# Kernel tuning notes

Measured on AMD Instinct MI355X. Metric: run time of the kernel, lower is better.

The kernel has to match this reference:

```python
import jax, jax.numpy as jnp
import numpy as np
import math

N_HEADS = 16

def _apply_rope(t, cos, sin):
    # t: [b, h, s, hd]; cos/sin: [s, hd//2] (interleaved pairs, llama2.c style)
    b, h, s, hd = t.shape
    tr = t.reshape(b, h, s, hd // 2, 2)
    x_r, x_i = tr[..., 0], tr[..., 1]
    c = cos[None, None, :, :]
    sn = sin[None, None, :, :]
    o_r = x_r * c - x_i * sn
    o_i = x_r * sn + x_i * c
    return jnp.stack([o_r, o_i], axis=-1).reshape(b, h, s, hd)

def setup_inputs() -> dict:
    key = jax.random.key(0)
    ks = jax.random.split(key, 7)
    b, s, d = 4, 2048, 2048
    hd = d // N_HEADS
    x = jax.random.normal(ks[0], (b, s, d), dtype=jnp.float32)
    # RoPE tables: cos/sin of theta * pos, standard 10000 base
    inv_freq = 1.0 / (10000.0 ** (np.arange(0, hd, 2, dtype=np.float32) / hd))
    pos = np.arange(s, dtype=np.float32)
    ang = np.outer(pos, inv_freq)  # [s, hd/2]
    freq_cos = jnp.asarray(np.cos(ang), dtype=jnp.float32)
    freq_sin = jnp.asarray(np.sin(ang), dtype=jnp.float32)
    Wqkv = jax.random.normal(ks[1], (d, 3 * d), dtype=jnp.float32) * (1.0 / math.sqrt(d))
    bqkv = jnp.zeros((3 * d,), dtype=jnp.float32)
    Wout = jax.random.normal(ks[2], (d, d), dtype=jnp.float32) * (1.0 / math.sqrt(d))
    bout = jnp.zeros((d,), dtype=jnp.float32)
    return {"x": x, "freq_cos": freq_cos, "freq_sin": freq_sin,
            "Wqkv": Wqkv, "bqkv": bqkv, "Wout": Wout, "bout": bout}

def reference(x, freq_cos, freq_sin, Wqkv, bqkv, Wout, bout):
    b, s, d = x.shape
    hd = d // N_HEADS
    qkv = x @ Wqkv + bqkv                       # [b, s, 3d]
    q, k, v = jnp.split(qkv, 3, axis=-1)
    def to_heads(t):
        return t.reshape(b, s, N_HEADS, hd).transpose(0, 2, 1, 3)  # [b, h, s, hd]
    q, k, v = to_heads(q), to_heads(k), to_heads(v)
    q = _apply_rope(q, freq_cos, freq_sin)
    k = _apply_rope(k, freq_cos, freq_sin)
    att = jnp.einsum('bhqd,bhkd->bhqk', q, k) / math.sqrt(hd)
    mask = jnp.tril(jnp.ones((s, s), dtype=bool))
    att = jnp.where(mask[None, None, :, :], att, -jnp.inf)
    att = jax.nn.softmax(att, axis=-1)
    y = jnp.einsum('bhqk,bhkd->bhqd', att, v)
    y = y.transpose(0, 2, 1, 3).reshape(b, s, d)
    return y @ Wout + bout
```

## Files before the change

kernel.cpp:

```cpp
#include <hip/hip_runtime.h>

typedef __attribute__((ext_vector_type(4))) float f32x4;
typedef __attribute__((ext_vector_type(8))) short bf16x8;
typedef __attribute__((ext_vector_type(4))) unsigned int uint4v;
typedef __attribute__((ext_vector_type(4))) unsigned short ushort4v;
typedef unsigned short u16;
typedef unsigned int u32;

#define AS1(p) ((const __attribute__((address_space(1))) u32*)(p))
#define AS3(p) ((__attribute__((address_space(3))) u32*)(p))

__device__ __forceinline__ float bf2f(u16 v) {
    u32 u = ((u32)v) << 16;
    return __builtin_bit_cast(float, u);
}
__device__ __forceinline__ u16 f2bf(float f) {
    u32 u = __builtin_bit_cast(u32, f);
    u += 0x7fffu + ((u >> 16) & 1u);
    return (u16)(u >> 16);
}

__global__ __launch_bounds__(256) void k_cvt_bf16(const float* __restrict__ in,
                                                  u16* __restrict__ out, int n8) {
    int t = blockIdx.x * 256 + threadIdx.x;
    if (t >= n8) return;
    const f32x4* p = (const f32x4*)in + (size_t)t * 2;
    f32x4 a = p[0], b = p[1];
    uint4v o;
    o[0] = (u32)f2bf(a[0]) | ((u32)f2bf(a[1]) << 16);
    o[1] = (u32)f2bf(a[2]) | ((u32)f2bf(a[3]) << 16);
    o[2] = (u32)f2bf(b[0]) | ((u32)f2bf(b[1]) << 16);
    o[3] = (u32)f2bf(b[2]) | ((u32)f2bf(b[3]) << 16);
    *((uint4v*)(out + (size_t)t * 8)) = o;
}

__global__ __launch_bounds__(256) void k_transpose_bf16(const float* __restrict__ in,
                                                        u16* __restrict__ out,
                                                        int R, int C) {
    __shared__ float tile[32][33];
    const int bx = blockIdx.x * 32, by = blockIdx.y * 32;
    const int tx = threadIdx.x & 31, ty = threadIdx.x >> 5;
#pragma unroll
    for (int i = 0; i < 32; i += 8)
        tile[ty + i][tx] = in[(size_t)(by + ty + i) * C + bx + tx];
    __syncthreads();
#pragma unroll
    for (int i = 0; i < 32; i += 8)
        out[(size_t)(bx + ty + i) * R + by + tx] = f2bf(tile[tx][ty + i]);
}

template <int OUT_BF16>
__global__ __launch_bounds__(512, 2) void k_gemm256(const u16* __restrict__ A,
                                                    const u16* __restrict__ Bt,
                                                    const float* __restrict__ bias,
                                                    void* __restrict__ Cout,
                                                    int M, int N, int K) {
    __shared__ u16 lds[65536];
    const int tid = threadIdx.x;
    const int wid = tid >> 6, l = tid & 63;
    const int lr = l & 15, lg = l >> 4;
    const int wm = wid >> 2, wn = wid & 3;
    const size_t brow = (size_t)blockIdx.x * 256;
    const size_t bcol = (size_t)blockIdx.y * 256;
    const int KT = K >> 5;

    const int srow = l & 15, scol = (l >> 4) * 8;
    const u16* gA0 = A  + (brow + (size_t)(2 * wid)     * 16 + srow) * K + scol;
    const u16* gA1 = A  + (brow + (size_t)(2 * wid + 1) * 16 + srow) * K + scol;
    const u16* gB0 = Bt + (bcol + (size_t)(2 * wid)     * 16 + srow) * K + scol;
    const u16* gB1 = Bt + (bcol + (size_t)(2 * wid + 1) * 16 + srow) * K + scol;

    f32x4 acc[8][4];
#pragma unroll
    for (int m = 0; m < 8; ++m)
#pragma unroll
        for (int n = 0; n < 4; ++n) acc[m][n] = (f32x4){0.f, 0.f, 0.f, 0.f};

#define STAGE(t)                                                                   \
    {                                                                              \
        const int b_ = (t) & 3;                                                    \
        const int k0_ = (t) << 5;                                                  \
        u16* dA_ = &lds[b_ * 8192 + (2 * wid) * 512];                              \
        u16* dB_ = &lds[32768 + b_ * 8192 + (2 * wid) * 512];                      \
        __builtin_amdgcn_global_load_lds(AS1(gA0 + k0_), AS3(dA_), 16, 0, 0);      \
        __builtin_amdgcn_global_load_lds(AS1(gA1 + k0_), AS3(dA_ + 512), 16, 0, 0);\
        __builtin_amdgcn_global_load_lds(AS1(gB0 + k0_), AS3(dB_), 16, 0, 0);      \
        __builtin_amdgcn_global_load_lds(AS1(gB1 + k0_), AS3(dB_ + 512), 16, 0, 0);\
    }

    STAGE(0); STAGE(1); STAGE(2);
    asm volatile("s_waitcnt vmcnt(8)" ::: "memory");
    __builtin_amdgcn_s_barrier();
    __builtin_amdgcn_sched_barrier(0);

#pragma unroll 1
    for (int t = 0; t < KT; ++t) {
        if (t + 3 < KT) STAGE(t + 3);
        const u16* pa = &lds[(t & 3) * 8192 + wm * 4096 + lg * 128 + lr * 8];
        const u16* pb = &lds[32768 + (t & 3) * 8192 + wn * 2048 + lg * 128 + lr * 8];
        bf16x8 af[8], bf[4];
#pragma unroll
        for (int m = 0; m < 8; ++m) af[m] = *(const bf16x8*)(pa + m * 512);
#pragma unroll
        for (int n = 0; n < 4; ++n) bf[n] = *(const bf16x8*)(pb + n * 512);
        __builtin_amdgcn_s_setprio(1);
#pragma unroll
        for (int m = 0; m < 8; ++m)
#pragma unroll
            for (int n = 0; n < 4; ++n)
                acc[m][n] = __builtin_amdgcn_mfma_f32_16x16x32_bf16(af[m], bf[n], acc[m][n], 0, 0, 0);
        __builtin_amdgcn_s_setprio(0);
        __builtin_amdgcn_sched_barrier(0);
        if (t < KT - 3)       asm volatile("s_waitcnt vmcnt(8)" ::: "memory");
        else if (t == KT - 3) asm volatile("s_waitcnt vmcnt(4)" ::: "memory");
        else if (t == KT - 2) asm volatile("s_waitcnt vmcnt(0)" ::: "memory");
        if (t < KT - 1) __builtin_amdgcn_s_barrier();
        __builtin_amdgcn_sched_barrier(0);
    }
#undef STAGE

    const int crow0 = wm * 128 + lg * 4;
    const int ccol0 = wn * 64 + lr;
#pragma unroll
    for (int m = 0; m < 8; ++m) {
        const size_t row0 = brow + crow0 + m * 16;
#pragma unroll
        for (int n = 0; n < 4; ++n) {
            const size_t col = bcol + ccol0 + n * 16;
            const float bv = bias[col];
#pragma unroll
            for (int r = 0; r < 4; ++r) {
                float v = acc[m][n][r] + bv;
                if (OUT_BF16)
                    ((u16*)Cout)[(row0 + r) * N + col] = f2bf(v);
                else
                    ((float*)Cout)[(row0 + r) * N + col] = v;
            }
        }
    }
}

__global__ __launch_bounds__(256) void k_rope(const u16* __restrict__ qkv,
                                              const float* __restrict__ fcos,
                                              const float* __restrict__ fsin,
                                              u16* __restrict__ qb, u16* __restrict__ kb) {
    const int t = blockIdx.x * 256 + threadIdx.x;
    const int e = t & 7, h = (t >> 3) & 15, r = (t >> 7) & 1, s = (t >> 8) & 2047, b = t >> 19;
    const u16* src = qkv + ((size_t)(b * 2048 + s)) * 6144 + r * 2048 + h * 128 + e * 16;
    uint4v p0 = *(const uint4v*)src;
    uint4v p1 = *(const uint4v*)(src + 8);
    const float* cp = fcos + s * 64 + e * 8;
    const float* sp = fsin + s * 64 + e * 8;
    f32x4 c0 = *(const f32x4*)cp, c1 = *(const f32x4*)(cp + 4);
    f32x4 s0 = *(const f32x4*)sp, s1 = *(const f32x4*)(sp + 4);
    float x[16];
#pragma unroll
    for (int i = 0; i < 4; ++i) {
        x[2 * i]     = bf2f((u16)(p0[i] & 0xffff));
        x[2 * i + 1] = bf2f((u16)(p0[i] >> 16));
        x[8 + 2 * i]     = bf2f((u16)(p1[i] & 0xffff));
        x[8 + 2 * i + 1] = bf2f((u16)(p1[i] >> 16));
    }
    float c[8]  = {c0[0], c0[1], c0[2], c0[3], c1[0], c1[1], c1[2], c1[3]};
    float sn[8] = {s0[0], s0[1], s0[2], s0[3], s1[0], s1[1], s1[2], s1[3]};
    u32 ow[8];
#pragma unroll
    for (int i = 0; i < 8; ++i) {
        float xr = x[2 * i], xi = x[2 * i + 1];
        float orr = xr * c[i] - xi * sn[i];
        float oii = xr * sn[i] + xi * c[i];
        ow[i] = (u32)f2bf(orr) | ((u32)f2bf(oii) << 16);
    }
    u16* dst = (r ? kb : qb) + ((size_t)((b * 16 + h) * 2048 + s)) * 128 + e * 16;
    uint4v q0 = {ow[0], ow[1], ow[2], ow[3]};
    uint4v q1 = {ow[4], ow[5], ow[6], ow[7]};
    *(uint4v*)dst = q0;
    *(uint4v*)(dst + 8) = q1;
}

struct VtRegs { uint4v v0, v1, v2, v3; };

__device__ __forceinline__ void attn_stage_k(const u16* kp, int kbase, u16* dstBase,
                                             int w, int lr, int lg) {
#pragma unroll
    for (int c = 0; c < 4; ++c) {
        const int row = w * 16 + c * 4 + lg;
        const int sslot = lr ^ (4 * (c & 1) + lg);
        const u16* gsrc = kp + (size_t)(kbase + row) * 128 + sslot * 8;
        __builtin_amdgcn_global_load_lds(AS1(gsrc), AS3(dstBase + (w * 16 + c * 4) * 128), 16, 0, 0);
    }
}

__device__ __forceinline__ VtRegs attn_load_v(const u16* vp, int kbase, int tid) {
    const int rg = tid >> 4, cg = tid & 15;
    const u16* gv = vp + (size_t)(kbase + rg * 4) * 6144 + cg * 8;
    VtRegs r;
    r.v0 = *(const uint4v*)gv;
    r.v1 = *(const uint4v*)(gv + 6144);
    r.v2 = *(const uint4v*)(gv + 2 * 6144);
    r.v3 = *(const uint4v*)(gv + 3 * 6144);
    return r;
}

__device__ __forceinline__ void attn_write_v(u16 (*Vt)[64], const VtRegs& r, int tid) {
    const int rg = tid >> 4, cg = tid & 15;
    const u16* u0 = (const u16*)&r.v0;
    const u16* u1 = (const u16*)&r.v1;
    const u16* u2 = (const u16*)&r.v2;
    const u16* u3 = (const u16*)&r.v3;
    const int sb = rg >> 1, hf = (rg & 1) * 4;
#pragma unroll
    for (int cc = 0; cc < 8; ++cc) {
        const int row = cg * 8 + cc;
        const int col = ((sb ^ ((cg ^ cc) & 7)) << 3) + hf;
        ushort4v pk = {u0[cc], u1[cc], u2[cc], u3[cc]};
        *(ushort4v*)&Vt[row][col] = pk;
    }
}

__device__ __forceinline__ void attn_qtile(int qt, const u16* qp, const u16* kp,
                                           const u16* vp, u16* yp,
                                           u16 (*Ks)[64][128], u16 (*Vt)[64],
                                           u16 (*Psw)[72],
                                           int w, int lr, int lg, int tid) {
    const int qw = qt * 128 + w * 32;

    bf16x8 qf[2][4];
#pragma unroll
    for (int i = 0; i < 2; ++i)
#pragma unroll
        for (int ks = 0; ks < 4; ++ks)
            qf[i][ks] = *(const bf16x8*)(qp + (size_t)(qw + i * 16 + lr) * 128 + ks * 32 + lg * 8);

    f32x4 acc[2][8];
#pragma unroll
    for (int i = 0; i < 2; ++i)
#pragma unroll
        for (int j = 0; j < 8; ++j) acc[i][j] = (f32x4){0.f, 0.f, 0.f, 0.f};
    float mrow[2][4], lrow[2][4];
#pragma unroll
    for (int i = 0; i < 2; ++i)
#pragma unroll
        for (int r = 0; r < 4; ++r) { mrow[i][r] = -1e30f; lrow[i][r] = 0.f; }

    const float scale = 0.08838834764831845f;
    const int nkt = 2 * qt + 2;

    attn_stage_k(kp, 0, &Ks[0][0][0], w, lr, lg);
    VtRegs vr = attn_load_v(vp, 0, tid);
    attn_write_v(Vt, vr, tid);
    __syncthreads();

    int cur = 0;
    for (int kt = 0; kt < nkt; ++kt) {
        const int kbase = kt * 64;
        const bool pf = (kt + 1 < nkt);
        if (pf) {
            attn_stage_k(kp, kbase + 64, &Ks[cur ^ 1][0][0], w, lr, lg);
            vr = attn_load_v(vp, kbase + 64, tid);
        }

        if (kbase <= qw + 31) {
            f32x4 sc[2][4];
#pragma unroll
            for (int i = 0; i < 2; ++i)
#pragma unroll
                for (int j = 0; j < 4; ++j) sc[i][j] = (f32x4){0.f, 0.f, 0.f, 0.f};
#pragma unroll
            for (int nt = 0; nt < 4; ++nt) {
#pragma unroll
                for (int ks = 0; ks < 4; ++ks) {
                    const int slot = (ks * 4 + lg) ^ (lr & 7);
                    bf16x8 kf = *(const bf16x8*)&Ks[cur][nt * 16 + lr][slot * 8];
#pragma unroll
                    for (int mt = 0; mt < 2; ++mt)
                        sc[mt][nt] = __builtin_amdgcn_mfma_f32_16x16x32_bf16(qf[mt][ks], kf, sc[mt][nt], 0, 0, 0);
                }
            }
            const bool pm = (kbase + 63 > qw);
#pragma unroll
            for (int mt = 0; mt < 2; ++mt)
#pragma unroll
                for (int nt = 0; nt < 4; ++nt)
#pragma unroll
                    for (int r = 0; r < 4; ++r) {
                        float v = sc[mt][nt][r] * scale;
                        if (pm) {
                            const int qi = qw + mt * 16 + lg * 4 + r;
                            const int ki = kbase + nt * 16 + lr;
                            if (ki > qi) v = -1e30f;
                        }
                        sc[mt][nt][r] = v;
                    }
            float rm[2][4];
#pragma unroll
            for (int mt = 0; mt < 2; ++mt)
#pragma unroll
                for (int r = 0; r < 4; ++r)
                    rm[mt][r] = fmaxf(fmaxf(sc[mt][0][r], sc[mt][1][r]),
                                      fmaxf(sc[mt][2][r], sc[mt][3][r]));
#pragma unroll
            for (int off = 8; off; off >>= 1)
#pragma unroll
                for (int mt = 0; mt < 2; ++mt)
#pragma unroll
                    for (int r = 0; r < 4; ++r)
                        rm[mt][r] = fmaxf(rm[mt][r], __shfl_xor(rm[mt][r], off, 16));
            float fac[2][4];
#pragma unroll
            for (int mt = 0; mt < 2; ++mt)
#pragma unroll
                for (int r = 0; r < 4; ++r) {
                    const float mn = fmaxf(mrow[mt][r], rm[mt][r]);
                    fac[mt][r] = __expf(mrow[mt][r] - mn);
                    mrow[mt][r] = mn;
                    lrow[mt][r] *= fac[mt][r];
                }
#pragma unroll
            for (int mt = 0; mt < 2; ++mt)
#pragma unroll
                for (int nt = 0; nt < 8; ++nt)
#pragma unroll
                    for (int r = 0; r < 4; ++r) acc[mt][nt][r] *= fac[mt][r];
            float rs[2][4] = {{0.f, 0.f, 0.f, 0.f}, {0.f, 0.f, 0.f, 0.f}};
#pragma unroll
            for (int mt = 0; mt < 2; ++mt)
#pragma unroll
                for (int nt = 0; nt < 4; ++nt)
#pragma unroll
                    for (int r = 0; r < 4; ++r) {
                        const float p = __expf(sc[mt][nt][r] - mrow[mt][r]);
                        sc[mt][nt][r] = p;
                        rs[mt][r] += p;
                    }
#pragma unroll
            for (int off = 8; off; off >>= 1)
#pragma unroll
                for (int mt = 0; mt < 2; ++mt)
#pragma unroll
                    for (int r = 0; r < 4; ++r)
                        rs[mt][r] += __shfl_xor(rs[mt][r], off, 16);
#pragma unroll
            for (int mt = 0; mt < 2; ++mt)
#pragma unroll
                for (int r = 0; r < 4; ++r) lrow[mt][r] += rs[mt][r];
#pragma unroll
            for (int mt = 0; mt < 2; ++mt)
#pragma unroll
                for (int nt = 0; nt < 4; ++nt)
#pragma unroll
                    for (int r = 0; r < 4; ++r)
                        Psw[mt * 16 + lg * 4 + r][nt * 16 + lr] = f2bf(sc[mt][nt][r]);
#pragma unroll
            for (int k2 = 0; k2 < 2; ++k2) {
                bf16x8 pa[2];
                pa[0] = *(const bf16x8*)&Psw[lr][k2 * 32 + lg * 8];
                pa[1] = *(const bf16x8*)&Psw[16 + lr][k2 * 32 + lg * 8];
#pragma unroll
                for (int nt = 0; nt < 8; ++nt) {
                    const int f = ((nt * 2 + (lr >> 3)) ^ lr) & 7;
                    const int slot = (k2 * 4 + lg) ^ f;
                    bf16x8 vb = *(const bf16x8*)&Vt[nt * 16 + lr][slot * 8];
#pragma unroll
                    for (int mt = 0; mt < 2; ++mt)
                        acc[mt][nt] = __builtin_amdgcn_mfma_f32_16x16x32_bf16(pa[mt], vb, acc[mt][nt], 0, 0, 0);
                }
            }
        }

        __syncthreads();
        if (pf) attn_write_v(Vt, vr, tid);
        __syncthreads();
        cur ^= 1;
    }

#pragma unroll
    for (int mt = 0; mt < 2; ++mt)
#pragma unroll
        for (int r = 0; r < 4; ++r) {
            const float inv = 1.f / lrow[mt][r];
            const size_t row = qw + mt * 16 + lg * 4 + r;
#pragma unroll
            for (int nt = 0; nt < 8; ++nt)
                yp[row * 2048 + nt * 16 + lr] = f2bf(acc[mt][nt][r] * inv);
        }
}

__global__ __launch_bounds__(256, 2) void k_attn(const u16* __restrict__ qb,
                                                 const u16* __restrict__ kb,
                                                 const u16* __restrict__ qkv,
                                                 u16* __restrict__ yb) {
    __shared__ u16 Ks[2][64][128];
    __shared__ u16 Vt[128][64];
    __shared__ u16 Ps[4][32][72];

    const int gid = blockIdx.x;
    const int x = gid >> 6;
    const int g = gid & 63;
    const int h = g & 15, b = g >> 4;
    const int tid = threadIdx.x;
    const int w = tid >> 6, l = tid & 63;
    const int lr = l & 15, lg = l >> 4;

    const u16* qp = qb + (size_t)((b * 16 + h) * 2048) * 128;
    const u16* kp = kb + (size_t)((b * 16 + h) * 2048) * 128;
    const u16* vp = qkv + (size_t)(b * 2048) * 6144 + 4096 + h * 128;
    u16* yp = yb + (size_t)(b * 2048) * 2048 + h * 128;

    attn_qtile(x,      qp, kp, vp, yp, Ks, Vt, Ps[w], w, lr, lg, tid);
    attn_qtile(15 - x, qp, kp, vp, yp, Ks, Vt, Ps[w], w, lr, lg, tid);
}

extern "C" void kernel_launch(void* const* d_in, const int* in_sizes, int n_in,
                              void* d_out, int out_size, void* d_ws, size_t ws_size,
                              hipStream_t stream) {
    const float* x    = (const float*)d_in[0];
    const float* fcos = (const float*)d_in[1];
    const float* fsin = (const float*)d_in[2];
    const float* Wqkv = (const float*)d_in[3];
    const float* bqkv = (const float*)d_in[4];
    const float* Wout = (const float*)d_in[5];
    const float* bout = (const float*)d_in[6];
    float* out = (float*)d_out;

    if (ws_size < 234881024u) return;

    char* ws = (char*)d_ws;
    u16* x_bf  = (u16*)(ws);
    u16* wqkvT = (u16*)(ws + 33554432);
    u16* woutT = (u16*)(ws + 58720256);
    u16* qkv   = (u16*)(ws + 67108864);
    u16* qb    = (u16*)(ws + 167772160);
    u16* kb    = (u16*)(ws + 201326592);
    u16* yb    = x_bf;

    k_cvt_bf16<<<8192, 256, 0, stream>>>(x, x_bf, 2097152);
    k_transpose_bf16<<<dim3(192, 64), 256, 0, stream>>>(Wqkv, wqkvT, 2048, 6144);
    k_transpose_bf16<<<dim3(64, 64), 256, 0, stream>>>(Wout, woutT, 2048, 2048);
    k_gemm256<1><<<dim3(32, 24), 512, 0, stream>>>(x_bf, wqkvT, bqkv, qkv, 8192, 6144, 2048);
    k_rope<<<8192, 256, 0, stream>>>(qkv, fcos, fsin, qb, kb);
    k_attn<<<512, 256, 0, stream>>>(qb, kb, qkv, yb);
    k_gemm256<0><<<dim3(32, 8), 512, 0, stream>>>(yb, woutT, bout, out, 8192, 2048, 2048);
}
```

Measured before the change: 555.7 us.

## Use 32x32 MFMA in GEMM and lazy rescaling with exp2 in attention

Rewrites the 256x256 GEMM tile to use 32x32x16 bf16 MFMAs with a new LDS staging layout, splitting the MFMA block into two halves around barriers, which reduces LDS fragment reads per FLOP. In the attention softmax it folds log2(e) into the scale, uses exp2f, and skips the online-softmax rescale of the accumulator unless the running max grows by more than a threshold (lazy rescaling). The GEMM change reorganizes the schedule and adds an extra barrier per iteration. Lazy rescaling risks precision only if skipped growth leads to large exponents, which the threshold bounds.

```diff
diff --git a/kernel.cpp b/kernel.cpp
--- a/kernel.cpp
+++ b/kernel.cpp
@@ -1,6 +1,7 @@
 #include <hip/hip_runtime.h>
 
 typedef __attribute__((ext_vector_type(4))) float f32x4;
+typedef __attribute__((ext_vector_type(16))) float f32x16;
 typedef __attribute__((ext_vector_type(8))) short bf16x8;
 typedef __attribute__((ext_vector_type(4))) unsigned int uint4v;
 typedef __attribute__((ext_vector_type(4))) unsigned short ushort4v;
@@ -58,34 +59,33 @@
     __shared__ u16 lds[65536];
     const int tid = threadIdx.x;
     const int wid = tid >> 6, l = tid & 63;
-    const int lr = l & 15, lg = l >> 4;
     const int wm = wid >> 2, wn = wid & 3;
     const size_t brow = (size_t)blockIdx.x * 256;
     const size_t bcol = (size_t)blockIdx.y * 256;
     const int KT = K >> 5;
 
-    const int srow = l & 15, scol = (l >> 4) * 8;
-    const u16* gA0 = A  + (brow + (size_t)(2 * wid)     * 16 + srow) * K + scol;
-    const u16* gA1 = A  + (brow + (size_t)(2 * wid + 1) * 16 + srow) * K + scol;
-    const u16* gB0 = Bt + (bcol + (size_t)(2 * wid)     * 16 + srow) * K + scol;
-    const u16* gB1 = Bt + (bcol + (size_t)(2 * wid + 1) * 16 + srow) * K + scol;
-
-    f32x4 acc[8][4];
-#pragma unroll
-    for (int m = 0; m < 8; ++m)
-#pragma unroll
-        for (int n = 0; n < 4; ++n) acc[m][n] = (f32x4){0.f, 0.f, 0.f, 0.f};
-
-#define STAGE(t)                                                                   \
-    {                                                                              \
-        const int b_ = (t) & 3;                                                    \
-        const int k0_ = (t) << 5;                                                  \
-        u16* dA_ = &lds[b_ * 8192 + (2 * wid) * 512];                              \
-        u16* dB_ = &lds[32768 + b_ * 8192 + (2 * wid) * 512];                      \
-        __builtin_amdgcn_global_load_lds(AS1(gA0 + k0_), AS3(dA_), 16, 0, 0);      \
-        __builtin_amdgcn_global_load_lds(AS1(gA1 + k0_), AS3(dA_ + 512), 16, 0, 0);\
-        __builtin_amdgcn_global_load_lds(AS1(gB0 + k0_), AS3(dB_), 16, 0, 0);      \
-        __builtin_amdgcn_global_load_lds(AS1(gB1 + k0_), AS3(dB_ + 512), 16, 0, 0);\
+    const int srow = l & 31, sk8 = (l >> 5) * 8;
+    const u16* gA = A  + (brow + (size_t)wid * 32 + srow) * K + sk8;
+    const u16* gB = Bt + (bcol + (size_t)wid * 32 + srow) * K + sk8;
+
+    f32x16 acc[4][2];
+#pragma unroll
+    for (int m = 0; m < 4; ++m)
+#pragma unroll
+        for (int n = 0; n < 2; ++n)
+#pragma unroll
+            for (int r = 0; r < 16; ++r) acc[m][n][r] = 0.f;
+
+#define STAGE(t)                                                                       \
+    {                                                                                  \
+        const int b_ = (t) & 3;                                                        \
+        const int k0_ = (t) << 5;                                                      \
+        u16* dA_ = &lds[b_ * 8192 + wid * 1024];                                       \
+        u16* dB_ = &lds[32768 + b_ * 8192 + wid * 1024];                               \
+        __builtin_amdgcn_global_load_lds(AS1(gA + k0_), AS3(dA_), 16, 0, 0);           \
+        __builtin_amdgcn_global_load_lds(AS1(gA + k0_ + 16), AS3(dA_ + 512), 16, 0, 0);\
+        __builtin_amdgcn_global_load_lds(AS1(gB + k0_), AS3(dB_), 16, 0, 0);           \
+        __builtin_amdgcn_global_load_lds(AS1(gB + k0_ + 16), AS3(dB_ + 512), 16, 0, 0);\
     }
 
     STAGE(0); STAGE(1); STAGE(2);
@@ -96,45 +96,65 @@
 #pragma unroll 1
     for (int t = 0; t < KT; ++t) {
         if (t + 3 < KT) STAGE(t + 3);
-        const u16* pa = &lds[(t & 3) * 8192 + wm * 4096 + lg * 128 + lr * 8];
-        const u16* pb = &lds[32768 + (t & 3) * 8192 + wn * 2048 + lg * 128 + lr * 8];
-        bf16x8 af[8], bf[4];
-#pragma unroll
-        for (int m = 0; m < 8; ++m) af[m] = *(const bf16x8*)(pa + m * 512);
-#pragma unroll
-        for (int n = 0; n < 4; ++n) bf[n] = *(const bf16x8*)(pb + n * 512);
-        __builtin_amdgcn_s_setprio(1);
-#pragma unroll
-        for (int m = 0; m < 8; ++m)
-#pragma unroll
-            for (int n = 0; n < 4; ++n)
-                acc[m][n] = __builtin_amdgcn_mfma_f32_16x16x32_bf16(af[m], bf[n], acc[m][n], 0, 0, 0);
-        __builtin_amdgcn_s_setprio(0);
-        __builtin_amdgcn_sched_barrier(0);
+        const u16* pa = &lds[(t & 3) * 8192 + wm * 4096 + l * 8];
+        const u16* pb = &lds[32768 + (t & 3) * 8192 + wn * 2048 + l * 8];
+        bf16x8 af[4][2], bf[2][2];
+#pragma unroll
+        for (int m = 0; m < 4; ++m)
+#pragma unroll
+            for (int h = 0; h < 2; ++h)
+                af[m][h] = *(const bf16x8*)(pa + m * 1024 + h * 512);
+#pragma unroll
+        for (int n = 0; n < 2; ++n)
+#pragma unroll
+            for (int h = 0; h < 2; ++h)
+                bf[n][h] = *(const bf16x8*)(pb + n * 1024 + h * 512);
         if (t < KT - 3)       asm volatile("s_waitcnt vmcnt(8)" ::: "memory");
         else if (t == KT - 3) asm volatile("s_waitcnt vmcnt(4)" ::: "memory");
         else if (t == KT - 2) asm volatile("s_waitcnt vmcnt(0)" ::: "memory");
-        if (t < KT - 1) __builtin_amdgcn_s_barrier();
+        __builtin_amdgcn_s_barrier();
         __builtin_amdgcn_sched_barrier(0);
+        __builtin_amdgcn_s_setprio(1);
+#pragma unroll
+        for (int m = 0; m < 2; ++m)
+#pragma unroll
+            for (int n = 0; n < 2; ++n)
+#pragma unroll
+                for (int h = 0; h < 2; ++h)
+                    acc[m][n] = __builtin_amdgcn_mfma_f32_32x32x16_bf16(af[m][h], bf[n][h], acc[m][n], 0, 0, 0);
+        __builtin_amdgcn_s_setprio(0);
+        __builtin_amdgcn_s_barrier();
+        __builtin_amdgcn_sched_barrier(0);
+        __builtin_amdgcn_s_setprio(1);
+#pragma unroll
+        for (int m = 2; m < 4; ++m)
+#pragma unroll
+            for (int n = 0; n < 2; ++n)
+#pragma unroll
+                for (int h = 0; h < 2; ++h)
+                    acc[m][n] = __builtin_amdgcn_mfma_f32_32x32x16_bf16(af[m][h], bf[n][h], acc[m][n], 0, 0, 0);
+        __builtin_amdgcn_s_setprio(0);
+        __builtin_amdgcn_sched_barrier(0);
     }
 #undef STAGE
 
-    const int crow0 = wm * 128 + lg * 4;
-    const int ccol0 = wn * 64 + lr;
-#pragma unroll
-    for (int m = 0; m < 8; ++m) {
-        const size_t row0 = brow + crow0 + m * 16;
-#pragma unroll
-        for (int n = 0; n < 4; ++n) {
-            const size_t col = bcol + ccol0 + n * 16;
+    const int rsub = 4 * (l >> 5);
+    const int csub = l & 31;
+#pragma unroll
+    for (int m = 0; m < 4; ++m) {
+        const size_t row0 = brow + wm * 128 + m * 32 + rsub;
+#pragma unroll
+        for (int n = 0; n < 2; ++n) {
+            const size_t col = bcol + wn * 64 + n * 32 + csub;
             const float bv = bias[col];
 #pragma unroll
-            for (int r = 0; r < 4; ++r) {
+            for (int r = 0; r < 16; ++r) {
+                const size_t row = row0 + (r & 3) + 8 * (r >> 2);
                 float v = acc[m][n][r] + bv;
                 if (OUT_BF16)
-                    ((u16*)Cout)[(row0 + r) * N + col] = f2bf(v);
+                    ((u16*)Cout)[row * N + col] = f2bf(v);
                 else
-                    ((float*)Cout)[(row0 + r) * N + col] = v;
+                    ((float*)Cout)[row * N + col] = v;
             }
         }
     }
@@ -243,7 +263,7 @@
 #pragma unroll
         for (int r = 0; r < 4; ++r) { mrow[i][r] = -1e30f; lrow[i][r] = 0.f; }
 
-    const float scale = 0.08838834764831845f;
+    const float scale2 = 0.08838834764831845f * 1.4426950408889634f;
     const int nkt = 2 * qt + 2;
 
     attn_stage_k(kp, 0, &Ks[0][0][0], w, lr, lg);
@@ -284,7 +304,7 @@
                 for (int nt = 0; nt < 4; ++nt)
 #pragma unroll
                     for (int r = 0; r < 4; ++r) {
-                        float v = sc[mt][nt][r] * scale;
+                        float v = sc[mt][nt][r] * scale2;
                         if (pm) {
                             const int qi = qw + mt * 16 + lg * 4 + r;
                             const int ki = kbase + nt * 16 + lr;
@@ -306,22 +326,25 @@
 #pragma unroll
                     for (int r = 0; r < 4; ++r)
                         rm[mt][r] = fmaxf(rm[mt][r], __shfl_xor(rm[mt][r], off, 16));
-            float fac[2][4];
-#pragma unroll
-            for (int mt = 0; mt < 2; ++mt)
-#pragma unroll
-                for (int r = 0; r < 4; ++r) {
-                    const float mn = fmaxf(mrow[mt][r], rm[mt][r]);
-                    fac[mt][r] = __expf(mrow[mt][r] - mn);
-                    mrow[mt][r] = mn;
-                    lrow[mt][r] *= fac[mt][r];
-                }
-#pragma unroll
-            for (int mt = 0; mt < 2; ++mt)
-#pragma unroll
-                for (int nt = 0; nt < 8; ++nt)
-#pragma unroll
-                    for (int r = 0; r < 4; ++r) acc[mt][nt][r] *= fac[mt][r];
+            float mx = -1e30f;
+#pragma unroll
+            for (int mt = 0; mt < 2; ++mt)
+#pragma unroll
+                for (int r = 0; r < 4; ++r)
+                    mx = fmaxf(mx, rm[mt][r] - mrow[mt][r]);
+            if (__any(mx > 11.5f)) {
+#pragma unroll
+                for (int mt = 0; mt < 2; ++mt)
+#pragma unroll
+                    for (int r = 0; r < 4; ++r) {
+                        const float mn = fmaxf(mrow[mt][r], rm[mt][r]);
+                        const float fac = exp2f(mrow[mt][r] - mn);
+                        mrow[mt][r] = mn;
+                        lrow[mt][r] *= fac;
+#pragma unroll
+                        for (int nt = 0; nt < 8; ++nt) acc[mt][nt][r] *= fac;
+                    }
+            }
             float rs[2][4] = {{0.f, 0.f, 0.f, 0.f}, {0.f, 0.f, 0.f, 0.f}};
 #pragma unroll
             for (int mt = 0; mt < 2; ++mt)
@@ -329,7 +352,7 @@
                 for (int nt = 0; nt < 4; ++nt)
 #pragma unroll
                     for (int r = 0; r < 4; ++r) {
-                        const float p = __expf(sc[mt][nt][r] - mrow[mt][r]);
+                        const float p = exp2f(sc[mt][nt][r] - mrow[mt][r]);
                         sc[mt][nt][r] = p;
                         rs[mt][r] += p;
                     }
```

New measurement: 583.2 us. 4.9% more time.

## Restructure GEMM to BK=64 double buffer; transpose attention scores for lane-local softmax

Applied to the files above, without the earlier changes.

The GEMM moves from a 4-stage BK=32 pipeline to a 2-stage BK=64 pipeline, with eight async global-to-LDS loads per stage and two MFMA k-substeps per iteration. This halves the number of barriers per K, but the prefetch depth drops to one stage. In attention, the QK^T MFMA operands are swapped so each lane holds one query row's scores. Row max and sum then need only two cross-lane shuffles, and the rescale factor and final normalizer are gathered with __shfl. The V load is issued before the K stage, and explicit vmcnt/lgkmcnt waits with raw s_barrier replace __syncthreads, so the V global load can overlap the K staging.

```diff
diff --git a/kernel.cpp b/kernel.cpp
--- a/kernel.cpp
+++ b/kernel.cpp
@@ -62,13 +62,17 @@
     const int wm = wid >> 2, wn = wid & 3;
     const size_t brow = (size_t)blockIdx.x * 256;
     const size_t bcol = (size_t)blockIdx.y * 256;
-    const int KT = K >> 5;
-
-    const int srow = l & 15, scol = (l >> 4) * 8;
-    const u16* gA0 = A  + (brow + (size_t)(2 * wid)     * 16 + srow) * K + scol;
-    const u16* gA1 = A  + (brow + (size_t)(2 * wid + 1) * 16 + srow) * K + scol;
-    const u16* gB0 = Bt + (bcol + (size_t)(2 * wid)     * 16 + srow) * K + scol;
-    const u16* gB1 = Bt + (bcol + (size_t)(2 * wid + 1) * 16 + srow) * K + scol;
+    const int KT = K >> 6;
+
+    const u16* gA[4];
+    const u16* gB[4];
+#pragma unroll
+    for (int r = 0; r < 4; ++r) {
+        const int P = r * 8 + wid, g = P >> 1, kh = P & 1;
+        const size_t off = (size_t)(g * 16 + lr) * K + kh * 32 + lg * 8;
+        gA[r] = A + brow * K + off;
+        gB[r] = Bt + bcol * K + off;
+    }
 
     f32x4 acc[8][4];
 #pragma unroll
@@ -76,57 +80,60 @@
 #pragma unroll
         for (int n = 0; n < 4; ++n) acc[m][n] = (f32x4){0.f, 0.f, 0.f, 0.f};
 
-#define STAGE(t)                                                                   \
-    {                                                                              \
-        const int b_ = (t) & 3;                                                    \
-        const int k0_ = (t) << 5;                                                  \
-        u16* dA_ = &lds[b_ * 8192 + (2 * wid) * 512];                              \
-        u16* dB_ = &lds[32768 + b_ * 8192 + (2 * wid) * 512];                      \
-        __builtin_amdgcn_global_load_lds(AS1(gA0 + k0_), AS3(dA_), 16, 0, 0);      \
-        __builtin_amdgcn_global_load_lds(AS1(gA1 + k0_), AS3(dA_ + 512), 16, 0, 0);\
-        __builtin_amdgcn_global_load_lds(AS1(gB0 + k0_), AS3(dB_), 16, 0, 0);      \
-        __builtin_amdgcn_global_load_lds(AS1(gB1 + k0_), AS3(dB_ + 512), 16, 0, 0);\
-    }
-
-    STAGE(0); STAGE(1); STAGE(2);
-    asm volatile("s_waitcnt vmcnt(8)" ::: "memory");
+#define STAGE(t)                                                                        \
+    do {                                                                                \
+        const int b_ = (t) & 1;                                                         \
+        const int k0_ = (t) << 6;                                                       \
+        u16* dA_ = &lds[b_ * 16384];                                                    \
+        u16* dB_ = &lds[32768 + b_ * 16384];                                            \
+        __builtin_amdgcn_global_load_lds(AS1(gA[0] + k0_), AS3(dA_ + (0 * 8 + wid) * 512), 16, 0, 0); \
+        __builtin_amdgcn_global_load_lds(AS1(gB[0] + k0_), AS3(dB_ + (0 * 8 + wid) * 512), 16, 0, 0); \
+        __builtin_amdgcn_global_load_lds(AS1(gA[1] + k0_), AS3(dA_ + (1 * 8 + wid) * 512), 16, 0, 0); \
+        __builtin_amdgcn_global_load_lds(AS1(gB[1] + k0_), AS3(dB_ + (1 * 8 + wid) * 512), 16, 0, 0); \
+        __builtin_amdgcn_global_load_lds(AS1(gA[2] + k0_), AS3(dA_ + (2 * 8 + wid) * 512), 16, 0, 0); \
+        __builtin_amdgcn_global_load_lds(AS1(gB[2] + k0_), AS3(dB_ + (2 * 8 + wid) * 512), 16, 0, 0); \
+        __builtin_amdgcn_global_load_lds(AS1(gA[3] + k0_), AS3(dA_ + (3 * 8 + wid) * 512), 16, 0, 0); \
+        __builtin_amdgcn_global_load_lds(AS1(gB[3] + k0_), AS3(dB_ + (3 * 8 + wid) * 512), 16, 0, 0); \
+    } while (0)
+
+    STAGE(0);
+    asm volatile("s_waitcnt vmcnt(0)" ::: "memory");
     __builtin_amdgcn_s_barrier();
     __builtin_amdgcn_sched_barrier(0);
 
 #pragma unroll 1
     for (int t = 0; t < KT; ++t) {
-        if (t + 3 < KT) STAGE(t + 3);
-        const u16* pa = &lds[(t & 3) * 8192 + wm * 4096 + lg * 128 + lr * 8];
-        const u16* pb = &lds[32768 + (t & 3) * 8192 + wn * 2048 + lg * 128 + lr * 8];
-        bf16x8 af[8], bf[4];
-#pragma unroll
-        for (int m = 0; m < 8; ++m) af[m] = *(const bf16x8*)(pa + m * 512);
-#pragma unroll
-        for (int n = 0; n < 4; ++n) bf[n] = *(const bf16x8*)(pb + n * 512);
-        __builtin_amdgcn_s_setprio(1);
-#pragma unroll
-        for (int m = 0; m < 8; ++m)
-#pragma unroll
-            for (int n = 0; n < 4; ++n)
-                acc[m][n] = __builtin_amdgcn_mfma_f32_16x16x32_bf16(af[m], bf[n], acc[m][n], 0, 0, 0);
-        __builtin_amdgcn_s_setprio(0);
+        if (t + 1 < KT) STAGE(t + 1);
+        const u16* pa = &lds[(t & 1) * 16384 + wm * 8192 + l * 8];
+        const u16* pb = &lds[32768 + (t & 1) * 16384 + wn * 4096 + l * 8];
+#pragma unroll
+        for (int ks = 0; ks < 2; ++ks) {
+            bf16x8 af[8], bfr[4];
+#pragma unroll
+            for (int m = 0; m < 8; ++m) af[m] = *(const bf16x8*)(pa + (m * 2 + ks) * 512);
+#pragma unroll
+            for (int n = 0; n < 4; ++n) bfr[n] = *(const bf16x8*)(pb + (n * 2 + ks) * 512);
+            __builtin_amdgcn_s_setprio(1);
+#pragma unroll
+            for (int m = 0; m < 8; ++m)
+#pragma unroll
+                for (int n = 0; n < 4; ++n)
+                    acc[m][n] = __builtin_amdgcn_mfma_f32_16x16x32_bf16(af[m], bfr[n], acc[m][n], 0, 0, 0);
+            __builtin_amdgcn_s_setprio(0);
+        }
         __builtin_amdgcn_sched_barrier(0);
-        if (t < KT - 3)       asm volatile("s_waitcnt vmcnt(8)" ::: "memory");
-        else if (t == KT - 3) asm volatile("s_waitcnt vmcnt(4)" ::: "memory");
-        else if (t == KT - 2) asm volatile("s_waitcnt vmcnt(0)" ::: "memory");
-        if (t < KT - 1) __builtin_amdgcn_s_barrier();
+        asm volatile("s_waitcnt vmcnt(0)" ::: "memory");
+        __builtin_amdgcn_s_barrier();
         __builtin_amdgcn_sched_barrier(0);
     }
 #undef STAGE
 
-    const int crow0 = wm * 128 + lg * 4;
-    const int ccol0 = wn * 64 + lr;
 #pragma unroll
     for (int m = 0; m < 8; ++m) {
-        const size_t row0 = brow + crow0 + m * 16;
+        const size_t row0 = brow + wm * 128 + m * 16 + lg * 4;
 #pragma unroll
         for (int n = 0; n < 4; ++n) {
-            const size_t col = bcol + ccol0 + n * 16;
+            const size_t col = bcol + wn * 64 + n * 16 + lr;
             const float bv = bias[col];
 #pragma unroll
             for (int r = 0; r < 4; ++r) {
@@ -224,6 +231,7 @@
                                            u16 (*Psw)[72],
                                            int w, int lr, int lg, int tid) {
     const int qw = qt * 128 + w * 32;
+    const int l = tid & 63;
 
     bf16x8 qf[2][4];
 #pragma unroll
@@ -237,17 +245,13 @@
     for (int i = 0; i < 2; ++i)
 #pragma unroll
         for (int j = 0; j < 8; ++j) acc[i][j] = (f32x4){0.f, 0.f, 0.f, 0.f};
-    float mrow[2][4], lrow[2][4];
-#pragma unroll
-    for (int i = 0; i < 2; ++i)
-#pragma unroll
-        for (int r = 0; r < 4; ++r) { mrow[i][r] = -1e30f; lrow[i][r] = 0.f; }
+    float mrow[2] = {-1e30f, -1e30f}, lrow[2] = {0.f, 0.f};
 
     const float scale = 0.08838834764831845f;
     const int nkt = 2 * qt + 2;
 
+    VtRegs vr = attn_load_v(vp, 0, tid);
     attn_stage_k(kp, 0, &Ks[0][0][0], w, lr, lg);
-    VtRegs vr = attn_load_v(vp, 0, tid);
     attn_write_v(Vt, vr, tid);
     __syncthreads();
 
@@ -256,16 +260,16 @@
         const int kbase = kt * 64;
         const bool pf = (kt + 1 < nkt);
         if (pf) {
+            vr = attn_load_v(vp, kbase + 64, tid);
             attn_stage_k(kp, kbase + 64, &Ks[cur ^ 1][0][0], w, lr, lg);
-            vr = attn_load_v(vp, kbase + 64, tid);
         }
 
         if (kbase <= qw + 31) {
-            f32x4 sc[2][4];
+            f32x4 st[2][4];
 #pragma unroll
             for (int i = 0; i < 2; ++i)
 #pragma unroll
-                for (int j = 0; j < 4; ++j) sc[i][j] = (f32x4){0.f, 0.f, 0.f, 0.f};
+                for (int j = 0; j < 4; ++j) st[i][j] = (f32x4){0.f, 0.f, 0.f, 0.f};
 #pragma unroll
             for (int nt = 0; nt < 4; ++nt) {
 #pragma unroll
@@ -274,7 +278,7 @@
                     bf16x8 kf = *(const bf16x8*)&Ks[cur][nt * 16 + lr][slot * 8];
 #pragma unroll
                     for (int mt = 0; mt < 2; ++mt)
-                        sc[mt][nt] = __builtin_amdgcn_mfma_f32_16x16x32_bf16(qf[mt][ks], kf, sc[mt][nt], 0, 0, 0);
+                        st[mt][nt] = __builtin_amdgcn_mfma_f32_16x16x32_bf16(kf, qf[mt][ks], st[mt][nt], 0, 0, 0);
                 }
             }
             const bool pm = (kbase + 63 > qw);
@@ -284,73 +288,67 @@
                 for (int nt = 0; nt < 4; ++nt)
 #pragma unroll
                     for (int r = 0; r < 4; ++r) {
-                        float v = sc[mt][nt][r] * scale;
+                        float v = st[mt][nt][r] * scale;
                         if (pm) {
-                            const int qi = qw + mt * 16 + lg * 4 + r;
-                            const int ki = kbase + nt * 16 + lr;
+                            const int qi = qw + mt * 16 + lr;
+                            const int ki = kbase + nt * 16 + lg * 4 + r;
                             if (ki > qi) v = -1e30f;
                         }
-                        sc[mt][nt][r] = v;
+                        st[mt][nt][r] = v;
                     }
-            float rm[2][4];
+            float rm[2], fac[2];
+#pragma unroll
+            for (int mt = 0; mt < 2; ++mt) {
+                float m0 = st[mt][0][0];
+#pragma unroll
+                for (int nt = 0; nt < 4; ++nt)
+#pragma unroll
+                    for (int r = 0; r < 4; ++r) m0 = fmaxf(m0, st[mt][nt][r]);
+                m0 = fmaxf(m0, __shfl_xor(m0, 16));
+                m0 = fmaxf(m0, __shfl_xor(m0, 32));
+                rm[mt] = m0;
+                const float mn = fmaxf(mrow[mt], m0);
+                fac[mt] = __expf(mrow[mt] - mn);
+                mrow[mt] = mn;
+                lrow[mt] *= fac[mt];
+            }
+            float facr[2][4];
 #pragma unroll
             for (int mt = 0; mt < 2; ++mt)
 #pragma unroll
                 for (int r = 0; r < 4; ++r)
-                    rm[mt][r] = fmaxf(fmaxf(sc[mt][0][r], sc[mt][1][r]),
-                                      fmaxf(sc[mt][2][r], sc[mt][3][r]));
-#pragma unroll
-            for (int off = 8; off; off >>= 1)
-#pragma unroll
-                for (int mt = 0; mt < 2; ++mt)
-#pragma unroll
-                    for (int r = 0; r < 4; ++r)
-                        rm[mt][r] = fmaxf(rm[mt][r], __shfl_xor(rm[mt][r], off, 16));
-            float fac[2][4];
+                    facr[mt][r] = __shfl(fac[mt], (l & 48) | (lg * 4 + r));
 #pragma unroll
             for (int mt = 0; mt < 2; ++mt)
 #pragma unroll
-                for (int r = 0; r < 4; ++r) {
-                    const float mn = fmaxf(mrow[mt][r], rm[mt][r]);
-                    fac[mt][r] = __expf(mrow[mt][r] - mn);
-                    mrow[mt][r] = mn;
-                    lrow[mt][r] *= fac[mt][r];
+                for (int nt = 0; nt < 8; ++nt)
+#pragma unroll
+                    for (int r = 0; r < 4; ++r) acc[mt][nt][r] *= facr[mt][r];
+#pragma unroll
+            for (int mt = 0; mt < 2; ++mt) {
+                float rs = 0.f;
+#pragma unroll
+                for (int nt = 0; nt < 4; ++nt)
+#pragma unroll
+                    for (int r = 0; r < 4; ++r) {
+                        const float p = __expf(st[mt][nt][r] - mrow[mt]);
+                        st[mt][nt][r] = p;
+                        rs += p;
+                    }
+                rs += __shfl_xor(rs, 16);
+                rs += __shfl_xor(rs, 32);
+                lrow[mt] += rs;
+            }
+#pragma unroll
+            for (int mt = 0; mt < 2; ++mt)
+#pragma unroll
+                for (int nt = 0; nt < 4; ++nt) {
+                    const u32 p01 = (u32)f2bf(st[mt][nt][0]) | ((u32)f2bf(st[mt][nt][1]) << 16);
+                    const u32 p23 = (u32)f2bf(st[mt][nt][2]) | ((u32)f2bf(st[mt][nt][3]) << 16);
+                    u16* dst = &Psw[mt * 16 + lr][nt * 16 + lg * 4];
+                    *(u32*)dst = p01;
+                    *(u32*)(dst + 2) = p23;
                 }
-#pragma unroll
-            for (int mt = 0; mt < 2; ++mt)
-#pragma unroll
-                for (int nt = 0; nt < 8; ++nt)
-#pragma unroll
-                    for (int r = 0; r < 4; ++r) acc[mt][nt][r] *= fac[mt][r];
-            float rs[2][4] = {{0.f, 0.f, 0.f, 0.f}, {0.f, 0.f, 0.f, 0.f}};
-#pragma unroll
-            for (int mt = 0; mt < 2; ++mt)
-#pragma unroll
-                for (int nt = 0; nt < 4; ++nt)
-#pragma unroll
-                    for (int r = 0; r < 4; ++r) {
-                        const float p = __expf(sc[mt][nt][r] - mrow[mt][r]);
-                        sc[mt][nt][r] = p;
-                        rs[mt][r] += p;
-                    }
-#pragma unroll
-            for (int off = 8; off; off >>= 1)
-#pragma unroll
-                for (int mt = 0; mt < 2; ++mt)
-#pragma unroll
-                    for (int r = 0; r < 4; ++r)
-                        rs[mt][r] += __shfl_xor(rs[mt][r], off, 16);
-#pragma unroll
-            for (int mt = 0; mt < 2; ++mt)
-#pragma unroll
-                for (int r = 0; r < 4; ++r) lrow[mt][r] += rs[mt][r];
-#pragma unroll
-            for (int mt = 0; mt < 2; ++mt)
-#pragma unroll
-                for (int nt = 0; nt < 4; ++nt)
-#pragma unroll
-                    for (int r = 0; r < 4; ++r)
-                        Psw[mt * 16 + lg * 4 + r][nt * 16 + lr] = f2bf(sc[mt][nt][r]);
 #pragma unroll
             for (int k2 = 0; k2 < 2; ++k2) {
                 bf16x8 pa[2];
@@ -368,9 +366,17 @@
             }
         }
 
-        __syncthreads();
-        if (pf) attn_write_v(Vt, vr, tid);
-        __syncthreads();
+        __builtin_amdgcn_s_barrier();
+        __builtin_amdgcn_sched_barrier(0);
+        if (pf) {
+            asm volatile("s_waitcnt vmcnt(4)" ::: "memory");
+            attn_write_v(Vt, vr, tid);
+            asm volatile("s_waitcnt vmcnt(0) lgkmcnt(0)" ::: "memory");
+        } else {
+            asm volatile("s_waitcnt vmcnt(0) lgkmcnt(0)" ::: "memory");
+        }
+        __builtin_amdgcn_s_barrier();
+        __builtin_amdgcn_sched_barrier(0);
         cur ^= 1;
     }
 
@@ -378,7 +384,8 @@
     for (int mt = 0; mt < 2; ++mt)
 #pragma unroll
         for (int r = 0; r < 4; ++r) {
-            const float inv = 1.f / lrow[mt][r];
+            const float lsum = __shfl(lrow[mt], (l & 48) | (lg * 4 + r));
+            const float inv = 1.f / lsum;
             const size_t row = qw + mt * 16 + lg * 4 + r;
 #pragma unroll
             for (int nt = 0; nt < 8; ++nt)
```

Measured after the change: 559.0 us. Within noise of the previous version (+0.6%).
